# Kernel tuning notes

Hardware: AMD Instinct MI355X
Metric: run time of the kernel (lower is better)

## Reference

```python
import jax, jax.numpy as jnp
import numpy as np

D_MODEL = 1024
NUM_HEADS = 16
HEAD_DIM = D_MODEL // NUM_HEADS
BATCH = 8
SEQ = 2048
LN_EPS = 1e-5


def setup_inputs() -> dict:
    rng = jax.random.key(0)
    ks = jax.random.split(rng, 16)
    s = 0.02  # init scale for weights
    w = lambda k: jax.random.normal(k, (D_MODEL, D_MODEL), jnp.float32) * s
    return {
        "query": jax.random.normal(ks[0], (BATCH, SEQ, D_MODEL), jnp.float32),
        "key": jax.random.normal(ks[1], (BATCH, SEQ, D_MODEL), jnp.float32),
        "value": jax.random.normal(ks[2], (BATCH, SEQ, D_MODEL), jnp.float32),
        "Wq": w(ks[3]), "bq": jnp.zeros((D_MODEL,), jnp.float32),
        "Wk": w(ks[4]), "bk": jnp.zeros((D_MODEL,), jnp.float32),
        "Wv": w(ks[5]), "bv": jnp.zeros((D_MODEL,), jnp.float32),
        "ln_g": jnp.ones((D_MODEL,), jnp.float32),
        "ln_b": jnp.zeros((D_MODEL,), jnp.float32),
        "Wo": w(ks[6]), "bo": jnp.zeros((D_MODEL,), jnp.float32),
    }


def reference(query, key, value, Wq, bq, Wk, bk, Wv, bv, ln_g, ln_b, Wo, bo):
    N, L, dm = query.shape
    H, Dh = NUM_HEADS, HEAD_DIM
    # projections + split heads -> (N, H, L, Dh), matching torch .view().transpose(1,2)
    q = (query @ Wq.T + bq).reshape(N, L, H, Dh).transpose(0, 2, 1, 3)
    k = (key   @ Wk.T + bk).reshape(N, L, H, Dh).transpose(0, 2, 1, 3)
    v = (value @ Wv.T + bv).reshape(N, L, H, Dh).transpose(0, 2, 1, 3)
    # Faithful to source: einsum 'nqhd,nkhd->nhqk' applied to ALREADY-transposed
    # (N,H,L,Dh) tensors => per-position head-to-head attention, energy (N, L, H, H).
    energy = jnp.einsum('nhld,ngld->nlhg', q, k)  # (N, L, H, H)
    attn = jax.nn.softmax(energy / jnp.sqrt(jnp.float32(dm)), axis=3)
    # source einsum 'nhql,nlhd->nqhd' on transposed v -> (N, H, L, Dh)
    out = jnp.einsum('nlhg,ngld->nhld', attn, v)
    out = out.transpose(0, 2, 1, 3).reshape(N, L, dm)
    # dropout is identity in eval mode
    mu = out.mean(axis=-1, keepdims=True)
    var = out.var(axis=-1, keepdims=True)
    out = (out - mu) / jnp.sqrt(var + LN_EPS) * ln_g + ln_b
    return out @ Wo.T + bo
```

## Files before the change

kernel.cpp:

```cpp
#include <hip/hip_runtime.h>
#include <cstdint>

#define TOKENS 16384
#define DMODEL 1024
#define NHEADS 16
#define HDIM   64

typedef __bf16  bf16x8 __attribute__((ext_vector_type(8)));
typedef ushort  u16x8  __attribute__((ext_vector_type(8)));
typedef ushort  u16x4  __attribute__((ext_vector_type(4)));
typedef float   f32x4  __attribute__((ext_vector_type(4)));

__device__ __forceinline__ ushort f2bf(float f) {
    union { float f; unsigned int i; } v; v.f = f;
    return (ushort)((v.i + 0x8000u) >> 16);
}
__device__ __forceinline__ f32x4 mfma16(bf16x8 a, bf16x8 b, f32x4 c) {
    return __builtin_amdgcn_mfma_f32_16x16x32_bf16(a, b, c, 0, 0, 0);
}
__device__ __forceinline__ void gload_lds16(const void* g, void* l) {
    __builtin_amdgcn_global_load_lds(
        (const __attribute__((address_space(1))) unsigned int*)(uintptr_t)g,
        (__attribute__((address_space(3))) unsigned int*)(uintptr_t)l,
        16, 0, 0);
}
union BU { u16x8 u; bf16x8 b; };

struct CvtArgs {
    const float* src[4];
    ushort*      dst[4];
};

__global__ __launch_bounds__(256) void cvt_f32_bf16(CvtArgs a)
{
    const float* __restrict__ s = a.src[blockIdx.y];
    ushort*      __restrict__ d = a.dst[blockIdx.y];
    const long i = ((long)blockIdx.x * 256 + threadIdx.x) * 8;
    const f32x4 v0 = *(const f32x4*)(s + i);
    const f32x4 v1 = *(const f32x4*)(s + i + 4);
    u16x8 p;
    #pragma unroll
    for (int j = 0; j < 4; j++) {
        p[j]     = f2bf(v0[j]);
        p[4 + j] = f2bf(v1[j]);
    }
    *(u16x8*)(d + i) = p;
}

#define BM 128
#define BN 128
#define BK 32

struct GemmArgs {
    const ushort* A[3];
    const ushort* W[3];
    const float*  Bi[3];
    void*         C[3];
};

template<int BF16OUT>
__global__ __launch_bounds__(256) void gemm_bt_bias(GemmArgs args, int N, int K)
{
    __shared__ __align__(16) ushort As[2][BM * BK];
    __shared__ __align__(16) ushort Bs[2][BN * BK];

    const int gx = gridDim.x, gy = gridDim.y;
    const int lin   = (blockIdx.z * gy + blockIdx.y) * gx + blockIdx.x;
    const int total = gx * gy * gridDim.z;
    const int cpx   = total >> 3;
    const int swz   = (lin & 7) * cpx + (lin >> 3);
    const int bz    = swz / (gx * gy);
    const int rem   = swz - bz * gx * gy;
    const int by    = rem / gx;
    const int bx    = rem - by * gx;

    const ushort* __restrict__ A  = args.A[bz];
    const ushort* __restrict__ W  = args.W[bz];
    const float*  __restrict__ Bi = args.Bi[bz];

    const int tid  = threadIdx.x;
    const int wave = tid >> 6;
    const int lane = tid & 63;
    const int wm = wave >> 1;
    const int wn = wave & 1;
    const long rowBase = (long)by * BM;
    const long colBase = (long)bx * BN;

    const int c0  = tid;
    const int c1  = tid + 256;
    const int r0s = c0 >> 2, k0s = (((c0 & 3) ^ ((c0 >> 3) & 3)) * 8);
    const int r1s = c1 >> 2, k1s = (((c1 & 3) ^ ((c1 >> 3) & 3)) * 8);

    const int fr  = lane & 15;
    const int fks = (((lane >> 4) ^ ((fr >> 1) & 3)) * 8);

    f32x4 acc[4][4];
    #pragma unroll
    for (int i = 0; i < 4; i++)
        #pragma unroll
        for (int j = 0; j < 4; j++)
            acc[i][j] = (f32x4){0.f, 0.f, 0.f, 0.f};

    auto STAGE = [&](int b, int kt) {
        gload_lds16(A + (rowBase + r0s) * (long)K + kt + k0s, &As[b][c0 * 8]);
        gload_lds16(A + (rowBase + r1s) * (long)K + kt + k1s, &As[b][c1 * 8]);
        gload_lds16(W + (colBase + r0s) * (long)K + kt + k0s, &Bs[b][c0 * 8]);
        gload_lds16(W + (colBase + r1s) * (long)K + kt + k1s, &Bs[b][c1 * 8]);
    };

    const int nt = K / BK;
    int cur = 0;
    STAGE(0, 0);
    __syncthreads();

    for (int t = 0; t < nt; ++t) {
        if (t + 1 < nt) STAGE(cur ^ 1, (t + 1) * BK);

        bf16x8 af[4], bfv[4];
        #pragma unroll
        for (int i = 0; i < 4; i++)
            af[i] = *(const bf16x8*)&As[cur][(wm * 64 + i * 16 + fr) * BK + fks];
        #pragma unroll
        for (int j = 0; j < 4; j++)
            bfv[j] = *(const bf16x8*)&Bs[cur][(wn * 64 + j * 16 + fr) * BK + fks];

        #pragma unroll
        for (int i = 0; i < 4; i++)
            #pragma unroll
            for (int j = 0; j < 4; j++)
                acc[i][j] = mfma16(af[i], bfv[j], acc[i][j]);

        __syncthreads();
        cur ^= 1;
    }

    const int qd = lane >> 4;
    #pragma unroll
    for (int j = 0; j < 4; j++) {
        const long col = colBase + wn * 64 + j * 16 + fr;
        const float bv = Bi[col];
        #pragma unroll
        for (int i = 0; i < 4; i++) {
            const long r0 = rowBase + wm * 64 + i * 16 + qd * 4;
            #pragma unroll
            for (int r = 0; r < 4; r++) {
                const float val = acc[i][j][r] + bv;
                if (BF16OUT)
                    ((ushort*)args.C[bz])[(r0 + r) * (long)N + col] = f2bf(val);
                else
                    ((float*)args.C[bz])[(r0 + r) * (long)N + col] = val;
            }
        }
    }
}

#define PMS 40

__global__ __launch_bounds__(256) void attn_ln_mfma(
    const ushort* __restrict__ Qp, const ushort* __restrict__ Kp,
    const ushort* __restrict__ Vp,
    const float* __restrict__ lng, const float* __restrict__ lnb,
    ushort* __restrict__ O)
{
    __shared__ __align__(16) ushort Vs[4][16 * 64];
    __shared__ __align__(16) ushort Pm[4][16 * PMS];

    const int tid  = threadIdx.x;
    const int w    = tid >> 6;
    const int lane = tid & 63;
    const long tok  = (long)blockIdx.x * 4 + w;
    const long base = tok * DMODEL;

    gload_lds16(Vp + base +       lane * 8, &Vs[w][      lane * 8]);
    gload_lds16(Vp + base + 512 + lane * 8, &Vs[w][512 + lane * 8]);

    *(u16x4*)&Pm[w][(lane & 15) * PMS + 16 + (lane >> 4) * 4] = (u16x4){0, 0, 0, 0};

    const int fr = lane & 15;
    const int fs = (lane >> 4) * 8;

    const bf16x8 aq0 = *(const bf16x8*)(Qp + base + fr * 64 + fs);
    const bf16x8 aq1 = *(const bf16x8*)(Qp + base + fr * 64 + fs + 32);
    const bf16x8 bk0 = *(const bf16x8*)(Kp + base + fr * 64 + fs);
    const bf16x8 bk1 = *(const bf16x8*)(Kp + base + fr * 64 + fs + 32);

    f32x4 e = (f32x4){0.f, 0.f, 0.f, 0.f};
    e = mfma16(aq0, bk0, e);
    e = mfma16(aq1, bk1, e);

    #pragma unroll
    for (int r = 0; r < 4; ++r) {
        const float x = e[r] * 0.03125f;
        float mx = x;
        #pragma unroll
        for (int m = 1; m < 16; m <<= 1) mx = fmaxf(mx, __shfl_xor(mx, m, 64));
        const float ex = __expf(x - mx);
        float sm = ex;
        #pragma unroll
        for (int m = 1; m < 16; m <<= 1) sm += __shfl_xor(sm, m, 64);
        Pm[w][((lane >> 4) * 4 + r) * PMS + fr] = f2bf(ex / sm);
    }

    __syncthreads();

    const bf16x8 pa = *(const bf16x8*)&Pm[w][fr * PMS + fs];

    f32x4 o[4];
    #pragma unroll
    for (int dblk = 0; dblk < 4; ++dblk) {
        BU bu; bu.u = (u16x8){0, 0, 0, 0, 0, 0, 0, 0};
        if (lane < 32) {
            #pragma unroll
            for (int j = 0; j < 8; ++j)
                bu.u[j] = Vs[w][(fs + j) * 64 + dblk * 16 + fr];
        }
        o[dblk] = mfma16(pa, bu.b, (f32x4){0.f, 0.f, 0.f, 0.f});
    }

    float s1 = 0.f, s2 = 0.f;
    #pragma unroll
    for (int dblk = 0; dblk < 4; ++dblk)
        #pragma unroll
        for (int r = 0; r < 4; ++r) { const float v = o[dblk][r]; s1 += v; s2 += v * v; }
    #pragma unroll
    for (int m = 1; m < 64; m <<= 1) {
        s1 += __shfl_xor(s1, m, 64);
        s2 += __shfl_xor(s2, m, 64);
    }
    const float mu   = s1 * (1.f / DMODEL);
    const float var  = s2 * (1.f / DMODEL) - mu * mu;
    const float rstd = rsqrtf(var + 1e-5f);

    #pragma unroll
    for (int dblk = 0; dblk < 4; ++dblk) {
        #pragma unroll
        for (int r = 0; r < 4; ++r) {
            const int h = (lane >> 4) * 4 + r;
            const int i = h * HDIM + dblk * 16 + fr;
            O[base + i] = f2bf((o[dblk][r] - mu) * rstd * lng[i] + lnb[i]);
        }
    }
}

extern "C" void kernel_launch(void* const* d_in, const int* in_sizes, int n_in,
                              void* d_out, int out_size, void* d_ws, size_t ws_size,
                              hipStream_t stream)
{
    const float* query = (const float*)d_in[0];
    const float* key   = (const float*)d_in[1];
    const float* value = (const float*)d_in[2];
    const float* Wq = (const float*)d_in[3];
    const float* bq = (const float*)d_in[4];
    const float* Wk = (const float*)d_in[5];
    const float* bk = (const float*)d_in[6];
    const float* Wv = (const float*)d_in[7];
    const float* bv = (const float*)d_in[8];
    const float* lng = (const float*)d_in[9];
    const float* lnb = (const float*)d_in[10];
    const float* Wo = (const float*)d_in[11];
    const float* bo = (const float*)d_in[12];
    float* out = (float*)d_out;

    const long WELEMS = (long)DMODEL * DMODEL;

    ushort* wq_b = (ushort*)d_ws;
    ushort* wk_b = wq_b + WELEMS;
    ushort* wv_b = wk_b + WELEMS;
    ushort* wo_b = wv_b + WELEMS;
    ushort* cbuf = wo_b + WELEMS;

    int NC = 1;
    while (NC < 128 &&
           (size_t)(8 * WELEMS) + (size_t)(TOKENS / NC) * DMODEL * 10 > ws_size)
        NC <<= 1;
    const int CM = TOKENS / NC;
    const size_t CE = (size_t)CM * DMODEL;

    ushort* qb = cbuf;
    ushort* kb = qb + CE;
    ushort* vb = kb + CE;
    ushort* qp = vb + CE;
    ushort* vp = qp + CE;

    {
        CvtArgs cw;
        cw.src[0] = Wq; cw.src[1] = Wk; cw.src[2] = Wv; cw.src[3] = Wo;
        cw.dst[0] = wq_b; cw.dst[1] = wk_b; cw.dst[2] = wv_b; cw.dst[3] = wo_b;
        cvt_f32_bf16<<<dim3((unsigned)(WELEMS / 2048), 4), 256, 0, stream>>>(cw);
    }

    for (int c = 0; c < NC; ++c) {
        const size_t off = (size_t)c * CE;
        ushort* kp = (ushort*)(out + off);

        {
            CvtArgs ci;
            ci.src[0] = query + off; ci.src[1] = key + off; ci.src[2] = value + off;
            ci.src[3] = query;
            ci.dst[0] = qb; ci.dst[1] = kb; ci.dst[2] = vb; ci.dst[3] = qb;
            cvt_f32_bf16<<<dim3((unsigned)(CE / 2048), 3), 256, 0, stream>>>(ci);
        }

        GemmArgs g1;
        g1.A[0] = qb;    g1.A[1] = kb;   g1.A[2] = vb;
        g1.W[0] = wq_b;  g1.W[1] = wk_b; g1.W[2] = wv_b;
        g1.Bi[0] = bq;   g1.Bi[1] = bk;  g1.Bi[2] = bv;
        g1.C[0] = qp;    g1.C[1] = kp;   g1.C[2] = vp;
        gemm_bt_bias<1><<<dim3(DMODEL / BN, CM / BM, 3), 256, 0, stream>>>(
            g1, DMODEL, DMODEL);

        attn_ln_mfma<<<CM / 4, 256, 0, stream>>>(qp, kp, vp, lng, lnb, qb);

        GemmArgs g2;
        g2.A[0] = g2.A[1] = g2.A[2] = qb;
        g2.W[0] = g2.W[1] = g2.W[2] = wo_b;
        g2.Bi[0] = g2.Bi[1] = g2.Bi[2] = bo;
        g2.C[0] = g2.C[1] = g2.C[2] = out + off;
        gemm_bt_bias<0><<<dim3(DMODEL / BN, CM / BM, 1), 256, 0, stream>>>(
            g2, DMODEL, DMODEL);
    }
}
```

Before: 463.9 us.

## Replace 128x128 GEMM with 256x256 tile, 4-stage LDS pipeline and 8 waves

Replaces the projection and output GEMM kernels with a 512-thread kernel that computes 256x256 tiles using a 4-slot LDS ring buffer. Loads are prefetched three stages ahead and interleaved with MFMA half-steps, using explicit vmcnt waits and s_setprio around MFMA bursts. The XCD-aware block swizzle is generalized to handle counts not divisible by 8. The aim is more operand reuse per global load and better overlap of memory with compute. The cost is higher LDS and register use per block, and fewer blocks, which hurts wave occupancy and tail balance. The chunk-count cap also drops to 64 so a chunk stays divisible by 256 rows.

```diff
diff --git a/kernel.cpp b/kernel.cpp
--- a/kernel.cpp
+++ b/kernel.cpp
@@ -47,9 +47,9 @@
     *(u16x8*)(d + i) = p;
 }
 
-#define BM 128
-#define BN 128
-#define BK 32
+#define BM2 256
+#define BN2 256
+#define BK2 32
 
 struct GemmArgs {
     const ushort* A[3];
@@ -58,21 +58,41 @@
     void*         C[3];
 };
 
+#define G256_READ_B(slot)                                                     \
+    { _Pragma("unroll")                                                       \
+      for (int n = 0; n < 4; ++n)                                             \
+          bf[n] = *(const bf16x8*)&Bs[slot][(wn * 64 + n * 16 + fr) * BK2 + fks]; }
+
+#define G256_READ_A(slot, mh)                                                 \
+    { _Pragma("unroll")                                                       \
+      for (int m = 0; m < 4; ++m)                                             \
+          af[m] = *(const bf16x8*)&As[slot][(wm * 128 + (mh) * 64 + m * 16 + fr) * BK2 + fks]; }
+
+#define G256_MFMA(mh)                                                         \
+    { __builtin_amdgcn_s_setprio(1);                                          \
+      _Pragma("unroll")                                                       \
+      for (int m = 0; m < 4; ++m)                                             \
+          _Pragma("unroll")                                                   \
+          for (int n = 0; n < 4; ++n)                                         \
+              acc[(mh) * 4 + m][n] = mfma16(af[m], bf[n], acc[(mh) * 4 + m][n]); \
+      __builtin_amdgcn_s_setprio(0); }
+
 template<int BF16OUT>
-__global__ __launch_bounds__(256) void gemm_bt_bias(GemmArgs args, int N, int K)
+__global__ __launch_bounds__(512) void gemm256(GemmArgs args, int N, int K)
 {
-    __shared__ __align__(16) ushort As[2][BM * BK];
-    __shared__ __align__(16) ushort Bs[2][BN * BK];
+    __shared__ __align__(16) ushort As[4][BM2 * BK2];
+    __shared__ __align__(16) ushort Bs[4][BN2 * BK2];
 
     const int gx = gridDim.x, gy = gridDim.y;
-    const int lin   = (blockIdx.z * gy + blockIdx.y) * gx + blockIdx.x;
-    const int total = gx * gy * gridDim.z;
-    const int cpx   = total >> 3;
-    const int swz   = (lin & 7) * cpx + (lin >> 3);
-    const int bz    = swz / (gx * gy);
-    const int rem   = swz - bz * gx * gy;
-    const int by    = rem / gx;
-    const int bx    = rem - by * gx;
+    const int lin = (blockIdx.z * gy + blockIdx.y) * gx + blockIdx.x;
+    const int nwg = gx * gy * gridDim.z;
+    const int q = nwg >> 3, r = nwg & 7;
+    const int xcd = lin & 7, loc = lin >> 3;
+    const int swz = (xcd < r ? xcd * (q + 1) : r * (q + 1) + (xcd - r) * q) + loc;
+    const int bz  = swz / (gx * gy);
+    const int rem = swz - bz * gx * gy;
+    const int by  = rem / gx;
+    const int bx  = rem - by * gx;
 
     const ushort* __restrict__ A  = args.A[bz];
     const ushort* __restrict__ W  = args.W[bz];
@@ -81,74 +101,106 @@
     const int tid  = threadIdx.x;
     const int wave = tid >> 6;
     const int lane = tid & 63;
-    const int wm = wave >> 1;
-    const int wn = wave & 1;
-    const long rowBase = (long)by * BM;
-    const long colBase = (long)bx * BN;
-
-    const int c0  = tid;
-    const int c1  = tid + 256;
-    const int r0s = c0 >> 2, k0s = (((c0 & 3) ^ ((c0 >> 3) & 3)) * 8);
-    const int r1s = c1 >> 2, k1s = (((c1 & 3) ^ ((c1 >> 3) & 3)) * 8);
+    const int wm = wave >> 2;
+    const int wn = wave & 3;
+    const long rowBase = (long)by * BM2;
+    const long colBase = (long)bx * BN2;
+
+    const int gA0 = tid, gA1 = tid + 512;
+    const long aOff0 = (long)(gA0 >> 2) * K + (((gA0 & 3) ^ ((gA0 >> 3) & 3)) * 8);
+    const long aOff1 = (long)(gA1 >> 2) * K + (((gA1 & 3) ^ ((gA1 >> 3) & 3)) * 8);
+    const ushort* Abase = A + rowBase * K;
+    const ushort* Wbase = W + colBase * K;
 
     const int fr  = lane & 15;
     const int fks = (((lane >> 4) ^ ((fr >> 1) & 3)) * 8);
 
-    f32x4 acc[4][4];
-    #pragma unroll
-    for (int i = 0; i < 4; i++)
-        #pragma unroll
-        for (int j = 0; j < 4; j++)
-            acc[i][j] = (f32x4){0.f, 0.f, 0.f, 0.f};
-
-    auto STAGE = [&](int b, int kt) {
-        gload_lds16(A + (rowBase + r0s) * (long)K + kt + k0s, &As[b][c0 * 8]);
-        gload_lds16(A + (rowBase + r1s) * (long)K + kt + k1s, &As[b][c1 * 8]);
-        gload_lds16(W + (colBase + r0s) * (long)K + kt + k0s, &Bs[b][c0 * 8]);
-        gload_lds16(W + (colBase + r1s) * (long)K + kt + k1s, &Bs[b][c1 * 8]);
+    f32x4 acc[8][4];
+    #pragma unroll
+    for (int m = 0; m < 8; ++m)
+        #pragma unroll
+        for (int n = 0; n < 4; ++n)
+            acc[m][n] = (f32x4){0.f, 0.f, 0.f, 0.f};
+
+    auto stageA = [&](int slot, int kt) {
+        gload_lds16(Abase + aOff0 + (long)kt * BK2, &As[slot][gA0 * 8]);
+        gload_lds16(Abase + aOff1 + (long)kt * BK2, &As[slot][gA1 * 8]);
     };
-
-    const int nt = K / BK;
-    int cur = 0;
-    STAGE(0, 0);
-    __syncthreads();
-
-    for (int t = 0; t < nt; ++t) {
-        if (t + 1 < nt) STAGE(cur ^ 1, (t + 1) * BK);
-
-        bf16x8 af[4], bfv[4];
-        #pragma unroll
-        for (int i = 0; i < 4; i++)
-            af[i] = *(const bf16x8*)&As[cur][(wm * 64 + i * 16 + fr) * BK + fks];
-        #pragma unroll
-        for (int j = 0; j < 4; j++)
-            bfv[j] = *(const bf16x8*)&Bs[cur][(wn * 64 + j * 16 + fr) * BK + fks];
-
-        #pragma unroll
-        for (int i = 0; i < 4; i++)
+    auto stageB = [&](int slot, int kt) {
+        gload_lds16(Wbase + aOff0 + (long)kt * BK2, &Bs[slot][gA0 * 8]);
+        gload_lds16(Wbase + aOff1 + (long)kt * BK2, &Bs[slot][gA1 * 8]);
+    };
+
+    const int nt = K / BK2;
+
+    stageA(0, 0); stageB(0, 0);
+    stageA(1, 1); stageB(1, 1);
+    stageA(2, 2); stageB(2, 2);
+    asm volatile("s_waitcnt vmcnt(8)" ::: "memory");
+    __builtin_amdgcn_s_barrier();
+
+    bf16x8 af[4], bf[4];
+
+    for (int X = 0; X < nt - 3; ++X) {
+        const int slot = X & 3, st = (X + 3) & 3;
+        G256_READ_B(slot);
+        G256_READ_A(slot, 0);
+        stageA(st, X + 3);
+        G256_MFMA(0);
+        __builtin_amdgcn_s_barrier();
+        G256_READ_A(slot, 1);
+        stageB(st, X + 3);
+        G256_MFMA(1);
+        asm volatile("s_waitcnt vmcnt(8)" ::: "memory");
+        __builtin_amdgcn_s_barrier();
+    }
+    {
+        const int slot = (nt - 3) & 3;
+        G256_READ_B(slot);
+        G256_READ_A(slot, 0);
+        G256_MFMA(0);
+        __builtin_amdgcn_s_barrier();
+        G256_READ_A(slot, 1);
+        G256_MFMA(1);
+        asm volatile("s_waitcnt vmcnt(4)" ::: "memory");
+        __builtin_amdgcn_s_barrier();
+    }
+    {
+        const int slot = (nt - 2) & 3;
+        G256_READ_B(slot);
+        G256_READ_A(slot, 0);
+        G256_MFMA(0);
+        __builtin_amdgcn_s_barrier();
+        G256_READ_A(slot, 1);
+        G256_MFMA(1);
+        asm volatile("s_waitcnt vmcnt(0)" ::: "memory");
+        __builtin_amdgcn_s_barrier();
+    }
+    {
+        const int slot = (nt - 1) & 3;
+        G256_READ_B(slot);
+        G256_READ_A(slot, 0);
+        G256_MFMA(0);
+        __builtin_amdgcn_s_barrier();
+        G256_READ_A(slot, 1);
+        G256_MFMA(1);
+    }
+
+    const int qd = lane >> 4;
+    #pragma unroll
+    for (int n = 0; n < 4; ++n) {
+        const long col = colBase + wn * 64 + n * 16 + fr;
+        const float bv = Bi[col];
+        #pragma unroll
+        for (int m = 0; m < 8; ++m) {
+            const long r0 = rowBase + wm * 128 + m * 16 + qd * 4;
             #pragma unroll
-            for (int j = 0; j < 4; j++)
-                acc[i][j] = mfma16(af[i], bfv[j], acc[i][j]);
-
-        __syncthreads();
-        cur ^= 1;
-    }
-
-    const int qd = lane >> 4;
-    #pragma unroll
-    for (int j = 0; j < 4; j++) {
-        const long col = colBase + wn * 64 + j * 16 + fr;
-        const float bv = Bi[col];
-        #pragma unroll
-        for (int i = 0; i < 4; i++) {
-            const long r0 = rowBase + wm * 64 + i * 16 + qd * 4;
-            #pragma unroll
-            for (int r = 0; r < 4; r++) {
-                const float val = acc[i][j][r] + bv;
+            for (int r2 = 0; r2 < 4; ++r2) {
+                const float val = acc[m][n][r2] + bv;
                 if (BF16OUT)
-                    ((ushort*)args.C[bz])[(r0 + r) * (long)N + col] = f2bf(val);
+                    ((ushort*)args.C[bz])[(r0 + r2) * (long)N + col] = f2bf(val);
                 else
-                    ((float*)args.C[bz])[(r0 + r) * (long)N + col] = val;
+                    ((float*)args.C[bz])[(r0 + r2) * (long)N + col] = val;
             }
         }
     }
@@ -270,7 +322,7 @@
     ushort* cbuf = wo_b + WELEMS;
 
     int NC = 1;
-    while (NC < 128 &&
+    while (NC < 64 &&
            (size_t)(8 * WELEMS) + (size_t)(TOKENS / NC) * DMODEL * 10 > ws_size)
         NC <<= 1;
     const int CM = TOKENS / NC;
@@ -306,7 +358,7 @@
         g1.W[0] = wq_b;  g1.W[1] = wk_b; g1.W[2] = wv_b;
         g1.Bi[0] = bq;   g1.Bi[1] = bk;  g1.Bi[2] = bv;
         g1.C[0] = qp;    g1.C[1] = kp;   g1.C[2] = vp;
-        gemm_bt_bias<1><<<dim3(DMODEL / BN, CM / BM, 3), 256, 0, stream>>>(
+        gemm256<1><<<dim3(DMODEL / BN2, CM / BM2, 3), 512, 0, stream>>>(
             g1, DMODEL, DMODEL);
 
         attn_ln_mfma<<<CM / 4, 256, 0, stream>>>(qp, kp, vp, lng, lnb, qb);
@@ -316,7 +368,7 @@
         g2.W[0] = g2.W[1] = g2.W[2] = wo_b;
         g2.Bi[0] = g2.Bi[1] = g2.Bi[2] = bo;
         g2.C[0] = g2.C[1] = g2.C[2] = out + off;
-        gemm_bt_bias<0><<<dim3(DMODEL / BN, CM / BM, 1), 256, 0, stream>>>(
+        gemm256<0><<<dim3(DMODEL / BN2, CM / BM2, 1), 512, 0, stream>>>(
             g2, DMODEL, DMODEL);
     }
 }
```

After: 432.0 us. 6.9% less time.
